# Kernel tuning notes

Hardware: AMD Instinct MI355X
Metric: run time of the kernel (lower is better)

Reference implementation:

```python
import jax, jax.numpy as jnp
import numpy as np

N_HEADS = 8
WINDOW = 7

def _conv1x1(x, W, b):
    # x: [B,H,W,C]; 1x1 conv == per-pixel matmul
    return jnp.einsum('bhwc,cd->bhwd', x, W) + b

def _to_heads(t, nh):
    # [B,H,W,C] -> channels-first reshape [B, nh, C//nh, H*W] (matches tf transpose+reshape)
    B, H, W, C = t.shape
    return jnp.transpose(t, (0, 3, 1, 2)).reshape(B, nh, C // nh, H * W)

def setup_inputs() -> dict:
    key = jax.random.key(0)
    ks = jax.random.split(key, 8)
    B, H, W, C = 2, 56, 56, 256
    x = jax.random.normal(ks[0], (B, H, W, C), dtype=jnp.float32)
    s = 1.0 / np.sqrt(C)
    Wq = jax.random.normal(ks[1], (C, C), dtype=jnp.float32) * s
    bq = jnp.zeros((C,), dtype=jnp.float32)
    Wk = jax.random.normal(ks[2], (C, C), dtype=jnp.float32) * s
    bk = jnp.zeros((C,), dtype=jnp.float32)
    Wv = jax.random.normal(ks[3], (C, C), dtype=jnp.float32) * s
    bv = jnp.zeros((C,), dtype=jnp.float32)
    # original initializes gamma to 0 (output == x); use small nonzero so the
    # attention path is observable in outputs/grads
    gamma = jax.random.normal(ks[4], (1,), dtype=jnp.float32) * 0.1
    return {"x": x, "Wq": Wq, "bq": bq, "Wk": Wk, "bk": bk, "Wv": Wv, "bv": bv, "gamma": gamma}

def reference(x, Wq, bq, Wk, bk, Wv, bv, gamma):
    B, H, W, C = x.shape
    p = WINDOW // 2
    xp = jnp.pad(x, ((0, 0), (p, p), (p, p), (0, 0)), mode='reflect')  # [B,Hp,Wp,C]
    q = _to_heads(_conv1x1(x, Wq, bq), N_HEADS)    # [B,nh,dk,HW]
    k = _to_heads(_conv1x1(xp, Wk, bk), N_HEADS)   # [B,nh,dk,HpWp]
    v = _to_heads(_conv1x1(xp, Wv, bv), N_HEADS)   # [B,nh,dk,HpWp]
    energy = jnp.einsum('bhdq,bhdk->bhqk', q, k)   # [B,nh,HW,HpWp]
    attn = jax.nn.softmax(energy, axis=-1)
    out = jnp.einsum('bhdk,bhqk->bhdq', v, attn)   # [B,nh,dk,HW]
    out = out.reshape(B, C, H, W).transpose(0, 2, 3, 1)
    return gamma * out + x
```

## Files before the change

kernel.cpp:

```cpp
#include <hip/hip_runtime.h>

typedef unsigned short u16;
typedef float f32x4 __attribute__((ext_vector_type(4)));
typedef short bf16x8 __attribute__((ext_vector_type(8)));

__device__ __forceinline__ u16 f2bf(float f) {
    unsigned u = __float_as_uint(f);
    u = (u + 0x7FFFu + ((u >> 16) & 1u)) >> 16;
    return (u16)u;
}

#define LOG2E 1.4426950408889634f

#if __has_builtin(__builtin_amdgcn_exp2f)
__device__ __forceinline__ float exp2_fast(float x) { return __builtin_amdgcn_exp2f(x); }
#else
__device__ __forceinline__ float exp2_fast(float x) { return __expf(x * 0.6931471805599453f); }
#endif

__device__ __forceinline__ unsigned pack2bf(float a, float b) {
    unsigned ua = __float_as_uint(a) + 0x8000u;
    unsigned ub = __float_as_uint(b) + 0x8000u;
#if __has_builtin(__builtin_amdgcn_perm)
    return __builtin_amdgcn_perm(ub, ua, 0x07060302u);
#else
    return ((ua >> 16) & 0xFFFFu) | (ub & 0xFFFF0000u);
#endif
}

#if __has_builtin(__builtin_amdgcn_cvt_pk_bf16_f32)
typedef __bf16 bf2_t __attribute__((ext_vector_type(2)));
__device__ __forceinline__ unsigned cvtpk(float a, float b) {
    bf2_t r = __builtin_amdgcn_cvt_pk_bf16_f32(a, b);
    return __builtin_bit_cast(unsigned, r);
}
#else
__device__ __forceinline__ unsigned cvtpk(float a, float b) { return pack2bf(a, b); }
#endif

__device__ __forceinline__ bf16x8 bc8(uint4 u) { return __builtin_bit_cast(bf16x8, u); }

#if __has_builtin(__builtin_amdgcn_global_load_lds)
typedef const __attribute__((address_space(1))) void* as1cv;
typedef __attribute__((address_space(3))) void* as3v;
__device__ __forceinline__ void dma16(const void* g, void* lds_base, int lane) {
    __builtin_amdgcn_global_load_lds((as1cv)g, (as3v)lds_base, 16, 0, 0);
}
#else
__device__ __forceinline__ void dma16(const void* g, void* lds_base, int lane) {
    *(uint4*)((char*)lds_base + lane * 16) = *(const uint4*)g;
}
#endif

#define BB 2
#define HH 56
#define SQ 3136
#define CROWN 3584

#define WS_Q    0
#define WS_K    1605632
#define WS_V    3244032
#define WS_WT   4882432
#define WS_CB   5079040
#define WS_XB   5082624

__global__ __launch_bounds__(256) void prep_kernel(const float* __restrict__ x,
                                                   const float* __restrict__ Wq,
                                                   const float* __restrict__ Wk,
                                                   const float* __restrict__ Wv,
                                                   u16* __restrict__ wtf,
                                                   u16* __restrict__ kbf,
                                                   u16* __restrict__ vbf,
                                                   u16* __restrict__ crow,
                                                   u16* __restrict__ xbf) {
    __shared__ __align__(16) char SM[17408];
    int tid = threadIdx.x;
    int bid = blockIdx.x;

    if (bid < 48) {
        u16 (*T)[68] = (u16(*)[68])SM;
        int mode = bid >> 4, rem = bid & 15;
        int kx = (rem >> 2) * 64, dx = (rem & 3) * 64;
        const float* W = (mode == 0) ? Wq : ((mode == 1) ? Wk : Wv);
        float sc = (mode == 0) ? LOG2E : 1.0f;
        int r16 = tid >> 4, c4 = (tid & 15) * 4;
#pragma unroll
        for (int p = 0; p < 4; ++p) {
            int kr = p * 16 + r16;
            float4 f = *(const float4*)&W[(size_t)(kx + kr) * 256 + dx + c4];
            T[kr][c4 + 0] = f2bf(f.x * sc);
            T[kr][c4 + 1] = f2bf(f.y * sc);
            T[kr][c4 + 2] = f2bf(f.z * sc);
            T[kr][c4 + 3] = f2bf(f.w * sc);
        }
        __syncthreads();
        int l16 = tid & 15, nt_loc = (tid >> 4) & 3, quad = (tid >> 6) & 3;
#pragma unroll
        for (int s_loc = 0; s_loc < 2; ++s_loc) {
            int k0 = s_loc * 32 + quad * 8;
            int d_loc = nt_loc * 16 + l16;
            u16 tmp[8];
#pragma unroll
            for (int j = 0; j < 8; ++j) tmp[j] = T[k0 + j][d_loc];
            int d = dx + d_loc;
            int nz = d >> 7, ntg = (d >> 4) & 7;
            int s = (kx >> 5) + s_loc;
            int f = (nz * 8 + s) * 8 + ntg;
            int L = quad * 16 + l16;
            *(uint4*)&wtf[(size_t)mode * 65536 + (size_t)f * 512 + (size_t)L * 8] = *(uint4*)tmp;
        }
        uint4 z4 = (uint4){0, 0, 0, 0};
        if (mode == 0 && kx == 0 && dx == 0) {
            for (int i = tid; i < 4096; i += 256) {
                int bb = i >> 11, rem2 = i & 2047;
                int t = 196 + (rem2 >> 9), off = (rem2 & 511) * 8;
                *(uint4*)&kbf[(((size_t)(bb * 200 + t)) << 12) + off] = z4;
            }
        }
        if (mode == 1 && kx == 0 && dx == 0) {
            for (int i = tid; i < CROWN; i += 256) {
                u16 v = 0;
                if (i < SQ) {
                    int rr = i / 56, cc = i - rr * 56;
                    int mr = (((rr >= 1) && (rr <= 3)) || ((rr >= 52) && (rr <= 54))) ? 2 : 1;
                    int mc = (((cc >= 1) && (cc <= 3)) || ((cc >= 52) && (cc <= 54))) ? 2 : 1;
                    int prod = mr * mc;
                    v = (prod == 1) ? (u16)0x3F80 : ((prod == 2) ? (u16)0x4000 : (u16)0x4080);
                }
                crow[i] = v;
            }
        }
        if (mode == 2 && kx == 0 && dx == 0) {
            for (int i = tid; i < 4096; i += 256) {
                int bh = i >> 8, rem2 = i & 255;
                int rgp = 196 + (rem2 >> 6), off = (rem2 & 63) * 8;
                *(uint4*)&vbf[(((size_t)(bh * 200 + rgp)) << 9) + off] = z4;
            }
        }
    } else {
        float (*T)[256] = (float(*)[256])SM;
        int tile = bid - 48;
        int r = tid >> 4, c0 = (tid & 15) * 16;
        const float* src = x + ((size_t)tile * 16 + r) * 256 + c0;
#pragma unroll
        for (int k = 0; k < 4; ++k)
            *(float4*)&T[r][c0 + k * 4] = *(const float4*)&src[k * 4];
        __syncthreads();
#pragma unroll
        for (int e = 0; e < 2; ++e) {
            int g = tid + e * 256;
            int s = g >> 6, L = g & 63;
            const float* row = &T[L & 15][s * 32 + (L >> 4) * 8];
            uint4 pk = (uint4){pack2bf(row[0], row[1]), pack2bf(row[2], row[3]),
                               pack2bf(row[4], row[5]), pack2bf(row[6], row[7])};
            *(uint4*)&xbf[(size_t)tile * 4096 + (size_t)g * 8] = pk;
        }
    }
}

__global__ __launch_bounds__(256, 4) void proj_kernel(const u16* __restrict__ xbf,
                                                      const u16* __restrict__ wtf,
                                                      const float* __restrict__ bq,
                                                      const float* __restrict__ bk,
                                                      const float* __restrict__ bv,
                                                      u16* __restrict__ qbf,
                                                      u16* __restrict__ kbf,
                                                      u16* __restrict__ vbf) {
    int mode = blockIdx.y, nz = blockIdx.z;
    int mbase = blockIdx.x * 64;
    int tid = threadIdx.x;
    int wave = tid >> 6, lane = tid & 63, quad = (tid >> 4) & 3, l16 = tid & 15;
    const float* bias = (mode == 0) ? bq : ((mode == 1) ? bk : bv);
    float wsc = (mode == 0) ? LOG2E : 1.0f;
    const u16* wf = wtf + (size_t)mode * 65536 + (size_t)nz * 32768 + (size_t)lane * 8;
    const u16* xt = xbf + (((size_t)(mbase >> 4) + wave) << 12);

    f32x4 acc[8];
#pragma unroll
    for (int i = 0; i < 8; i++) acc[i] = (f32x4){0.f, 0.f, 0.f, 0.f};

#pragma unroll
    for (int s = 0; s < 8; ++s) {
        bf16x8 af = *(const bf16x8*)&xt[(s << 9) + lane * 8];
        if (mode == 2) {
#pragma unroll
            for (int nt = 0; nt < 8; nt++) {
                bf16x8 bfrag = *(const bf16x8*)&wf[(s * 8 + nt) * 512];
                acc[nt] = __builtin_amdgcn_mfma_f32_16x16x32_bf16(af, bfrag, acc[nt], 0, 0, 0);
            }
        } else {
#pragma unroll
            for (int nt = 0; nt < 8; nt++) {
                bf16x8 bfrag = *(const bf16x8*)&wf[(s * 8 + nt) * 512];
                acc[nt] = __builtin_amdgcn_mfma_f32_16x16x32_bf16(bfrag, af, acc[nt], 0, 0, 0);
            }
        }
    }

    if (mode == 2) {
        int b_ = (mbase >= SQ) ? 1 : 0;
        int kp0 = mbase - b_ * SQ + wave * 16 + quad * 4;
        int rg = (mbase - b_ * SQ + wave * 16) >> 4;
        float mult[4];
#pragma unroll
        for (int p = 0; p < 4; ++p) {
            int kp = kp0 + p;
            int rr = kp / 56, cc = kp - rr * 56;
            float mr = (((rr >= 1) && (rr <= 3)) || ((rr >= 52) && (rr <= 54))) ? 2.f : 1.f;
            float mc = (((cc >= 1) && (cc <= 3)) || ((cc >= 52) && (cc <= 54))) ? 2.f : 1.f;
            mult[p] = mr * mc;
        }
#pragma unroll
        for (int nt = 0; nt < 8; nt++) {
            int c = nz * 128 + nt * 16 + l16;
            float bvv = bias[c];
            int h_idx = nz * 4 + (nt >> 1);
            int L = (nt & 1) * 16 + l16 + ((quad >> 1) & 1) * 32;
            float va0 = (acc[nt][0] + bvv) * mult[0];
            float va1 = (acc[nt][1] + bvv) * mult[1];
            float va2 = (acc[nt][2] + bvv) * mult[2];
            float va3 = (acc[nt][3] + bvv) * mult[3];
            uint2 pk = (uint2){pack2bf(va0, va1), pack2bf(va2, va3)};
            *(uint2*)&vbf[(((size_t)((b_ * 8 + h_idx) * 200 + rg)) << 9) + L * 8 + (quad & 1) * 4] = pk;
        }
    } else {
        u16* outp = (mode == 0) ? qbf : kbf;
        int t = (mbase >> 4) + wave;
        int tt = (mode == 0) ? t : (t + (t >= 196 ? 4 : 0));
#pragma unroll
        for (int nt = 0; nt < 8; nt++) {
            int c0 = nz * 128 + nt * 16 + quad * 4;
            float4 b4 = *(const float4*)&bias[c0];
            float v0 = acc[nt][0] + b4.x * wsc;
            float v1 = acc[nt][1] + b4.y * wsc;
            float v2 = acc[nt][2] + b4.z * wsc;
            float v3 = acc[nt][3] + b4.w * wsc;
            int s_idx = nz * 4 + (nt >> 1);
            int Lrow = ((nt & 1) * 2 + (quad >> 1)) * 16 + l16;
            uint2 pk = (uint2){pack2bf(v0, v1), pack2bf(v2, v3)};
            *(uint2*)&outp[(((size_t)(tt * 8 + s_idx)) << 9) + Lrow * 8 + (quad & 1) * 4] = pk;
        }
    }
}

__global__ __launch_bounds__(512, 6) void attn_kernel(const u16* __restrict__ qb,
                                                      const u16* __restrict__ kb,
                                                      const u16* __restrict__ vtb,
                                                      const u16* __restrict__ crow,
                                                      const float* __restrict__ x,
                                                      const float* __restrict__ gammap,
                                                      float* __restrict__ out,
                                                      int bh_base) {
    __shared__ __align__(16) u16 S[19968];

    int tid = threadIdx.x;
    int w = tid >> 6, lane = tid & 63, quad = lane >> 4, l16 = lane & 15;
    int g = w & 3, qh = w >> 2;
    int bh = bh_base + blockIdx.x;
    int b = bh >> 3, h = bh & 7;

    int qtile = b * 196 + blockIdx.y * 4 + qh * 2;
    bf16x8 qf[2];
#pragma unroll
    for (int i = 0; i < 2; ++i)
        qf[i] = *(const bf16x8*)&qb[(((size_t)(qtile + i) * 8 + h) << 9) + lane * 8];

    const u16* kg = kb + ((size_t)(b * 200) << 12);
    const u16* vg = vtb + (((size_t)((b * 8 + h) * 200)) << 9);

    f32x4 o[2][2], lv[2];
#pragma unroll
    for (int i = 0; i < 2; ++i) {
        o[i][0] = (f32x4){0.f, 0.f, 0.f, 0.f};
        o[i][1] = (f32x4){0.f, 0.f, 0.f, 0.f};
        lv[i]   = (f32x4){0.f, 0.f, 0.f, 0.f};
    }

    auto stage = [&](int r_ch, int buf) {
        u16* base = &S[buf * 8192];
        int rg = r_ch * 8 + w;
        dma16(kg + (((size_t)rg * 8 + h) << 9) + lane * 8, base + w * 512, lane);
        dma16(vg + (((size_t)rg) << 9) + lane * 8, base + 4096 + w * 512, lane);
    };

    int tA = g, tB = g + 4;
    int vOffA = tA * 512 + (((quad >> 1) * 32 + l16) << 3) + (quad & 1) * 4;
    int vOffB = tB * 512 + (((quad >> 1) * 32 + l16) << 3) + (quad & 1) * 4;

    auto round_body = [&](int r, int bR) {
        const u16* Kl = &S[bR * 8192];
        const u16* Vl = Kl + 4096;
        const u16* cnt = &S[16384] + r * 128;
        f32x4 z = (f32x4){0.f, 0.f, 0.f, 0.f};

        float pA[2][4];
        {
            bf16x8 kfA = *(const bf16x8*)&Kl[tA * 512 + lane * 8];
            f32x4 eA0 = __builtin_amdgcn_mfma_f32_16x16x32_bf16(kfA, qf[0], z, 0, 0, 0);
            f32x4 eA1 = __builtin_amdgcn_mfma_f32_16x16x32_bf16(kfA, qf[1], z, 0, 0, 0);
#pragma unroll
            for (int j = 0; j < 4; ++j) pA[0][j] = exp2_fast(eA0[j]);
#pragma unroll
            for (int j = 0; j < 4; ++j) pA[1][j] = exp2_fast(eA1[j]);
        }
        float pB[2][4];
        {
            bf16x8 kfB = *(const bf16x8*)&Kl[tB * 512 + lane * 8];
            f32x4 eB0 = __builtin_amdgcn_mfma_f32_16x16x32_bf16(kfB, qf[0], z, 0, 0, 0);
            f32x4 eB1 = __builtin_amdgcn_mfma_f32_16x16x32_bf16(kfB, qf[1], z, 0, 0, 0);
#pragma unroll
            for (int j = 0; j < 4; ++j) pB[0][j] = exp2_fast(eB0[j]);
#pragma unroll
            for (int j = 0; j < 4; ++j) pB[1][j] = exp2_fast(eB1[j]);
        }
        uint2 ca = *(const uint2*)&cnt[tA * 16 + quad * 4];
        uint2 cc = *(const uint2*)&cnt[tB * 16 + quad * 4];
        bf16x8 cf = bc8((uint4){ca.x, ca.y, cc.x, cc.y});
        uint2 wA0 = *(const uint2*)&Vl[vOffA];
        uint2 wB0 = *(const uint2*)&Vl[vOffB];
        bf16x8 V0 = bc8((uint4){wA0.x, wA0.y, wB0.x, wB0.y});
        uint2 wA1 = *(const uint2*)&Vl[vOffA + 128];
        uint2 wB1 = *(const uint2*)&Vl[vOffB + 128];
        bf16x8 V1 = bc8((uint4){wA1.x, wA1.y, wB1.x, wB1.y});

#pragma unroll
        for (int i = 0; i < 2; ++i) {
            bf16x8 pa = bc8((uint4){cvtpk(pA[i][0], pA[i][1]), cvtpk(pA[i][2], pA[i][3]),
                                    cvtpk(pB[i][0], pB[i][1]), cvtpk(pB[i][2], pB[i][3])});
            o[i][0] = __builtin_amdgcn_mfma_f32_16x16x32_bf16(pa, V0, o[i][0], 0, 0, 0);
            o[i][1] = __builtin_amdgcn_mfma_f32_16x16x32_bf16(pa, V1, o[i][1], 0, 0, 0);
            lv[i]   = __builtin_amdgcn_mfma_f32_16x16x32_bf16(pa, cf, lv[i], 0, 0, 0);
        }
    };

    if (w < 7) dma16(crow + w * 512 + lane * 8, (char*)&S[16384] + w * 1024, lane);
    stage(0, 0);

    for (int r = 0; r < 25; ++r) {
        asm volatile("s_waitcnt vmcnt(0)" ::: "memory");
        __builtin_amdgcn_s_barrier();
        asm volatile("" ::: "memory");
        if (r + 1 < 25) stage(r + 1, (r + 1) & 1);
        round_body(r, r & 1);
    }
    __syncthreads();

    float* mg = (float*)&S[0];
    {
        int slot = ((qh * 2 + (g & 1)) * 64 + lane) * 24;
        if (g >= 2) {
            *(f32x4*)&mg[slot + 0]  = o[0][0];
            *(f32x4*)&mg[slot + 4]  = o[0][1];
            *(f32x4*)&mg[slot + 8]  = o[1][0];
            *(f32x4*)&mg[slot + 12] = o[1][1];
            *(f32x4*)&mg[slot + 16] = lv[0];
            *(f32x4*)&mg[slot + 20] = lv[1];
        }
        __syncthreads();
        if (g < 2) {
            o[0][0] += *(const f32x4*)&mg[slot + 0];
            o[0][1] += *(const f32x4*)&mg[slot + 4];
            o[1][0] += *(const f32x4*)&mg[slot + 8];
            o[1][1] += *(const f32x4*)&mg[slot + 12];
            lv[0]   += *(const f32x4*)&mg[slot + 16];
            lv[1]   += *(const f32x4*)&mg[slot + 20];
        }
        __syncthreads();
    }
    {
        int slot = (qh * 64 + lane) * 24;
        if (g == 1) {
            *(f32x4*)&mg[slot + 0]  = o[0][0];
            *(f32x4*)&mg[slot + 4]  = o[0][1];
            *(f32x4*)&mg[slot + 8]  = o[1][0];
            *(f32x4*)&mg[slot + 12] = o[1][1];
            *(f32x4*)&mg[slot + 16] = lv[0];
            *(f32x4*)&mg[slot + 20] = lv[1];
        }
        __syncthreads();
        if (g == 0) {
            o[0][0] += *(const f32x4*)&mg[slot + 0];
            o[0][1] += *(const f32x4*)&mg[slot + 4];
            o[1][0] += *(const f32x4*)&mg[slot + 8];
            o[1][1] += *(const f32x4*)&mg[slot + 12];
            lv[0]   += *(const f32x4*)&mg[slot + 16];
            lv[1]   += *(const f32x4*)&mg[slot + 20];
            float gam = gammap[0];
#pragma unroll
            for (int i = 0; i < 2; ++i) {
#pragma unroll
                for (int r2 = 0; r2 < 4; ++r2) {
                    float scl = gam / lv[i][r2];
                    int q = blockIdx.y * 64 + qh * 32 + i * 16 + quad * 4 + r2;
                    size_t base = ((size_t)(b * SQ + q) << 8) + h * 32 + l16;
                    out[base]      = o[i][0][r2] * scl + x[base];
                    out[base + 16] = o[i][1][r2] * scl + x[base + 16];
                }
            }
        }
    }
}

extern "C" void kernel_launch(void* const* d_in, const int* in_sizes, int n_in,
                              void* d_out, int out_size, void* d_ws, size_t ws_size,
                              hipStream_t stream) {
    const float* x     = (const float*)d_in[0];
    const float* Wq    = (const float*)d_in[1];
    const float* bq    = (const float*)d_in[2];
    const float* Wk    = (const float*)d_in[3];
    const float* bk    = (const float*)d_in[4];
    const float* Wv    = (const float*)d_in[5];
    const float* bv    = (const float*)d_in[6];
    const float* gamma = (const float*)d_in[7];
    float* out = (float*)d_out;

    u16* ws   = (u16*)d_ws;
    u16* qbf  = ws + WS_Q;
    u16* kbf  = ws + WS_K;
    u16* vbf  = ws + WS_V;
    u16* wtf  = ws + WS_WT;
    u16* crow = ws + WS_CB;
    u16* xbf  = ws + WS_XB;

    prep_kernel<<<440, 256, 0, stream>>>(x, Wq, Wk, Wv, wtf, kbf, vbf, crow, xbf);
    proj_kernel<<<dim3(98, 3, 2), 256, 0, stream>>>(xbf, wtf, bq, bk, bv, qbf, kbf, vbf);
    attn_kernel<<<dim3(8, 49), 512, 0, stream>>>(qbf, kbf, vbf, crow, x, gamma, out, 0);
    attn_kernel<<<dim3(8, 49), 512, 0, stream>>>(qbf, kbf, vbf, crow, x, gamma, out, 8);
}
```

Measured before the change: 136.5 us.

## Make each attention wave own its K/V tiles and all four query tiles

The attention kernel moves from 512 threads to 256 threads per block. Each wave now computes all four 16-row query tiles against the K/V tiles that it stages itself. Because every wave only reads LDS data it loaded, the per-round block barrier is replaced by a per-wave vmcnt wait, which lets the next-round loads overlap compute without cross-wave sync. The two half-grid launches become one 16x49 launch, and MFMA sections are wrapped in s_setprio. The cost is more accumulator registers per wave (4 query tiles instead of 2) and a lower occupancy hint, which may reduce latency hiding.

```diff
diff --git a/kernel.cpp b/kernel.cpp
--- a/kernel.cpp
+++ b/kernel.cpp
@@ -243,47 +243,48 @@
     }
 }
 
-__global__ __launch_bounds__(512, 6) void attn_kernel(const u16* __restrict__ qb,
+__global__ __launch_bounds__(256, 4) void attn_kernel(const u16* __restrict__ qb,
                                                       const u16* __restrict__ kb,
                                                       const u16* __restrict__ vtb,
                                                       const u16* __restrict__ crow,
                                                       const float* __restrict__ x,
                                                       const float* __restrict__ gammap,
-                                                      float* __restrict__ out,
-                                                      int bh_base) {
+                                                      float* __restrict__ out) {
     __shared__ __align__(16) u16 S[19968];
 
     int tid = threadIdx.x;
     int w = tid >> 6, lane = tid & 63, quad = lane >> 4, l16 = lane & 15;
-    int g = w & 3, qh = w >> 2;
-    int bh = bh_base + blockIdx.x;
+    int bh = blockIdx.x;
     int b = bh >> 3, h = bh & 7;
-
-    int qtile = b * 196 + blockIdx.y * 4 + qh * 2;
-    bf16x8 qf[2];
-#pragma unroll
-    for (int i = 0; i < 2; ++i)
+    int qsub = blockIdx.y * 64;
+
+    int qtile = b * 196 + blockIdx.y * 4;
+    bf16x8 qf[4];
+#pragma unroll
+    for (int i = 0; i < 4; ++i)
         qf[i] = *(const bf16x8*)&qb[(((size_t)(qtile + i) * 8 + h) << 9) + lane * 8];
 
     const u16* kg = kb + ((size_t)(b * 200) << 12);
     const u16* vg = vtb + (((size_t)((b * 8 + h) * 200)) << 9);
 
-    f32x4 o[2][2], lv[2];
-#pragma unroll
-    for (int i = 0; i < 2; ++i) {
+    f32x4 o[4][2], lv[4];
+#pragma unroll
+    for (int i = 0; i < 4; ++i) {
         o[i][0] = (f32x4){0.f, 0.f, 0.f, 0.f};
         o[i][1] = (f32x4){0.f, 0.f, 0.f, 0.f};
         lv[i]   = (f32x4){0.f, 0.f, 0.f, 0.f};
     }
 
+    int tA = w, tB = w + 4;
     auto stage = [&](int r_ch, int buf) {
         u16* base = &S[buf * 8192];
-        int rg = r_ch * 8 + w;
-        dma16(kg + (((size_t)rg * 8 + h) << 9) + lane * 8, base + w * 512, lane);
-        dma16(vg + (((size_t)rg) << 9) + lane * 8, base + 4096 + w * 512, lane);
+        int rgA = r_ch * 8 + tA, rgB = r_ch * 8 + tB;
+        dma16(kg + (((size_t)rgA * 8 + h) << 9) + lane * 8, base + tA * 512, lane);
+        dma16(kg + (((size_t)rgB * 8 + h) << 9) + lane * 8, base + tB * 512, lane);
+        dma16(vg + (((size_t)rgA) << 9) + lane * 8, base + 4096 + tA * 512, lane);
+        dma16(vg + (((size_t)rgB) << 9) + lane * 8, base + 4096 + tB * 512, lane);
     };
 
-    int tA = g, tB = g + 4;
     int vOffA = tA * 512 + (((quad >> 1) * 32 + l16) << 3) + (quad & 1) * 4;
     int vOffB = tB * 512 + (((quad >> 1) * 32 + l16) << 3) + (quad & 1) * 4;
 
@@ -292,26 +293,35 @@
         const u16* Vl = Kl + 4096;
         const u16* cnt = &S[16384] + r * 128;
         f32x4 z = (f32x4){0.f, 0.f, 0.f, 0.f};
-
-        float pA[2][4];
+        unsigned paw[4][4];
+
         {
             bf16x8 kfA = *(const bf16x8*)&Kl[tA * 512 + lane * 8];
-            f32x4 eA0 = __builtin_amdgcn_mfma_f32_16x16x32_bf16(kfA, qf[0], z, 0, 0, 0);
-            f32x4 eA1 = __builtin_amdgcn_mfma_f32_16x16x32_bf16(kfA, qf[1], z, 0, 0, 0);
-#pragma unroll
-            for (int j = 0; j < 4; ++j) pA[0][j] = exp2_fast(eA0[j]);
-#pragma unroll
-            for (int j = 0; j < 4; ++j) pA[1][j] = exp2_fast(eA1[j]);
-        }
-        float pB[2][4];
+            f32x4 eA[4];
+            __builtin_amdgcn_s_setprio(1);
+#pragma unroll
+            for (int i = 0; i < 4; ++i)
+                eA[i] = __builtin_amdgcn_mfma_f32_16x16x32_bf16(kfA, qf[i], z, 0, 0, 0);
+            __builtin_amdgcn_s_setprio(0);
+#pragma unroll
+            for (int i = 0; i < 4; ++i) {
+                paw[i][0] = cvtpk(exp2_fast(eA[i][0]), exp2_fast(eA[i][1]));
+                paw[i][1] = cvtpk(exp2_fast(eA[i][2]), exp2_fast(eA[i][3]));
+            }
+        }
         {
             bf16x8 kfB = *(const bf16x8*)&Kl[tB * 512 + lane * 8];
-            f32x4 eB0 = __builtin_amdgcn_mfma_f32_16x16x32_bf16(kfB, qf[0], z, 0, 0, 0);
-            f32x4 eB1 = __builtin_amdgcn_mfma_f32_16x16x32_bf16(kfB, qf[1], z, 0, 0, 0);
-#pragma unroll
-            for (int j = 0; j < 4; ++j) pB[0][j] = exp2_fast(eB0[j]);
-#pragma unroll
-            for (int j = 0; j < 4; ++j) pB[1][j] = exp2_fast(eB1[j]);
+            f32x4 eB[4];
+            __builtin_amdgcn_s_setprio(1);
+#pragma unroll
+            for (int i = 0; i < 4; ++i)
+                eB[i] = __builtin_amdgcn_mfma_f32_16x16x32_bf16(kfB, qf[i], z, 0, 0, 0);
+            __builtin_amdgcn_s_setprio(0);
+#pragma unroll
+            for (int i = 0; i < 4; ++i) {
+                paw[i][2] = cvtpk(exp2_fast(eB[i][0]), exp2_fast(eB[i][1]));
+                paw[i][3] = cvtpk(exp2_fast(eB[i][2]), exp2_fast(eB[i][3]));
+            }
         }
         uint2 ca = *(const uint2*)&cnt[tA * 16 + quad * 4];
         uint2 cc = *(const uint2*)&cnt[tB * 16 + quad * 4];
@@ -323,75 +333,80 @@
         uint2 wB1 = *(const uint2*)&Vl[vOffB + 128];
         bf16x8 V1 = bc8((uint4){wA1.x, wA1.y, wB1.x, wB1.y});
 
-#pragma unroll
-        for (int i = 0; i < 2; ++i) {
-            bf16x8 pa = bc8((uint4){cvtpk(pA[i][0], pA[i][1]), cvtpk(pA[i][2], pA[i][3]),
-                                    cvtpk(pB[i][0], pB[i][1]), cvtpk(pB[i][2], pB[i][3])});
+        __builtin_amdgcn_s_setprio(1);
+#pragma unroll
+        for (int i = 0; i < 4; ++i) {
+            bf16x8 pa = bc8((uint4){paw[i][0], paw[i][1], paw[i][2], paw[i][3]});
             o[i][0] = __builtin_amdgcn_mfma_f32_16x16x32_bf16(pa, V0, o[i][0], 0, 0, 0);
             o[i][1] = __builtin_amdgcn_mfma_f32_16x16x32_bf16(pa, V1, o[i][1], 0, 0, 0);
             lv[i]   = __builtin_amdgcn_mfma_f32_16x16x32_bf16(pa, cf, lv[i], 0, 0, 0);
         }
+        __builtin_amdgcn_s_setprio(0);
     };
 
-    if (w < 7) dma16(crow + w * 512 + lane * 8, (char*)&S[16384] + w * 1024, lane);
+    {
+        dma16(crow + w * 512 + lane * 8, (char*)&S[16384] + w * 1024, lane);
+        if (w + 4 < 7)
+            dma16(crow + (w + 4) * 512 + lane * 8, (char*)&S[16384] + (w + 4) * 1024, lane);
+    }
     stage(0, 0);
+    __syncthreads();
 
     for (int r = 0; r < 25; ++r) {
-        asm volatile("s_waitcnt vmcnt(0)" ::: "memory");
-        __builtin_amdgcn_s_barrier();
-        asm volatile("" ::: "memory");
-        if (r + 1 < 25) stage(r + 1, (r + 1) & 1);
+        if (r + 1 < 25) {
+            stage(r + 1, (r + 1) & 1);
+            asm volatile("s_waitcnt vmcnt(4)" ::: "memory");
+        } else {
+            asm volatile("s_waitcnt vmcnt(0)" ::: "memory");
+        }
         round_body(r, r & 1);
     }
     __syncthreads();
 
     float* mg = (float*)&S[0];
     {
-        int slot = ((qh * 2 + (g & 1)) * 64 + lane) * 24;
-        if (g >= 2) {
-            *(f32x4*)&mg[slot + 0]  = o[0][0];
-            *(f32x4*)&mg[slot + 4]  = o[0][1];
-            *(f32x4*)&mg[slot + 8]  = o[1][0];
-            *(f32x4*)&mg[slot + 12] = o[1][1];
-            *(f32x4*)&mg[slot + 16] = lv[0];
-            *(f32x4*)&mg[slot + 20] = lv[1];
+        int slot = ((w & 1) * 64 + lane) * 48;
+        if (w >= 2) {
+#pragma unroll
+            for (int i = 0; i < 4; ++i) {
+                *(f32x4*)&mg[slot + i * 8]      = o[i][0];
+                *(f32x4*)&mg[slot + i * 8 + 4]  = o[i][1];
+                *(f32x4*)&mg[slot + 32 + i * 4] = lv[i];
+            }
         }
         __syncthreads();
-        if (g < 2) {
-            o[0][0] += *(const f32x4*)&mg[slot + 0];
-            o[0][1] += *(const f32x4*)&mg[slot + 4];
-            o[1][0] += *(const f32x4*)&mg[slot + 8];
-            o[1][1] += *(const f32x4*)&mg[slot + 12];
-            lv[0]   += *(const f32x4*)&mg[slot + 16];
-            lv[1]   += *(const f32x4*)&mg[slot + 20];
+        if (w < 2) {
+#pragma unroll
+            for (int i = 0; i < 4; ++i) {
+                o[i][0] += *(const f32x4*)&mg[slot + i * 8];
+                o[i][1] += *(const f32x4*)&mg[slot + i * 8 + 4];
+                lv[i]   += *(const f32x4*)&mg[slot + 32 + i * 4];
+            }
         }
         __syncthreads();
     }
     {
-        int slot = (qh * 64 + lane) * 24;
-        if (g == 1) {
-            *(f32x4*)&mg[slot + 0]  = o[0][0];
-            *(f32x4*)&mg[slot + 4]  = o[0][1];
-            *(f32x4*)&mg[slot + 8]  = o[1][0];
-            *(f32x4*)&mg[slot + 12] = o[1][1];
-            *(f32x4*)&mg[slot + 16] = lv[0];
-            *(f32x4*)&mg[slot + 20] = lv[1];
+        int slot = lane * 48;
+        if (w == 1) {
+#pragma unroll
+            for (int i = 0; i < 4; ++i) {
+                *(f32x4*)&mg[slot + i * 8]      = o[i][0];
+                *(f32x4*)&mg[slot + i * 8 + 4]  = o[i][1];
+                *(f32x4*)&mg[slot + 32 + i * 4] = lv[i];
+            }
         }
         __syncthreads();
-        if (g == 0) {
-            o[0][0] += *(const f32x4*)&mg[slot + 0];
-            o[0][1] += *(const f32x4*)&mg[slot + 4];
-            o[1][0] += *(const f32x4*)&mg[slot + 8];
-            o[1][1] += *(const f32x4*)&mg[slot + 12];
-            lv[0]   += *(const f32x4*)&mg[slot + 16];
-            lv[1]   += *(const f32x4*)&mg[slot + 20];
+        if (w == 0) {
             float gam = gammap[0];
 #pragma unroll
-            for (int i = 0; i < 2; ++i) {
+            for (int i = 0; i < 4; ++i) {
+                o[i][0] += *(const f32x4*)&mg[slot + i * 8];
+                o[i][1] += *(const f32x4*)&mg[slot + i * 8 + 4];
+                lv[i]   += *(const f32x4*)&mg[slot + 32 + i * 4];
 #pragma unroll
                 for (int r2 = 0; r2 < 4; ++r2) {
                     float scl = gam / lv[i][r2];
-                    int q = blockIdx.y * 64 + qh * 32 + i * 16 + quad * 4 + r2;
+                    int q = qsub + i * 16 + quad * 4 + r2;
                     size_t base = ((size_t)(b * SQ + q) << 8) + h * 32 + l16;
                     out[base]      = o[i][0][r2] * scl + x[base];
                     out[base + 16] = o[i][1][r2] * scl + x[base + 16];
@@ -424,6 +439,5 @@
 
     prep_kernel<<<440, 256, 0, stream>>>(x, Wq, Wk, Wv, wtf, kbf, vbf, crow, xbf);
     proj_kernel<<<dim3(98, 3, 2), 256, 0, stream>>>(xbf, wtf, bq, bk, bv, qbf, kbf, vbf);
-    attn_kernel<<<dim3(8, 49), 512, 0, stream>>>(qbf, kbf, vbf, crow, x, gamma, out, 0);
-    attn_kernel<<<dim3(8, 49), 512, 0, stream>>>(qbf, kbf, vbf, crow, x, gamma, out, 8);
-}
+    attn_kernel<<<dim3(16, 49), 256, 0, stream>>>(qbf, kbf, vbf, crow, x, gamma, out);
+}
```

Result: faster. 128.3 us (-6.1%).
